# Optimization experiments

Measured on AMD Instinct MI355X. Metric: run time of the kernel, lower is better.

The kernel has to match this reference:

```python
import jax, jax.numpy as jnp
import numpy as np

N = 50000      # nodes
E = 800000     # edges (avg degree 16)
F_IN = 64      # node_features (== GENConv out, so no input projection)
H = 64         # hidden
EXP = 2 * H    # GENConv MLP expansion dim = 128
D2 = F_IN + H  # dense-block concat dim = SAGEConv in = 128
EPS_MSG = 1e-7 # GENConv message eps
BN_EPS = 1e-5


def setup_inputs() -> dict:
    key = jax.random.key(0)
    ks = jax.random.split(key, 16)
    g = lambda k, shape, fan: jax.random.normal(k, shape, jnp.float32) / np.sqrt(fan)
    return {
        "x": jax.random.normal(ks[0], (N, F_IN), jnp.float32),
        "edge_index": jax.random.randint(ks[1], (2, E), 0, N, jnp.int32),
        # GENConv MLP: Linear(64,128) -> BatchNorm(128) -> ReLU -> Linear(128,64)
        "W1": g(ks[2], (H, EXP), H), "b1": jnp.zeros((EXP,), jnp.float32),
        "gamma": jnp.ones((EXP,), jnp.float32), "beta": jnp.zeros((EXP,), jnp.float32),
        "W2": g(ks[3], (EXP, H), EXP), "b2": jnp.zeros((H,), jnp.float32),
        # SAGEConv project Linear(128,128), lin_l Linear(128,64), lin_r Linear(128,64,bias=False)
        "Wp": g(ks[4], (D2, D2), D2), "bp": jnp.zeros((D2,), jnp.float32),
        "Wl": g(ks[5], (D2, H), D2), "bl": jnp.zeros((H,), jnp.float32),
        "Wr": g(ks[6], (D2, H), D2),
        # fc Linear(64,1)
        "Wf": g(ks[7], (H, 1), H), "bf": jnp.zeros((1,), jnp.float32),
    }


def _forward(x, W1, b1, gamma, beta, W2, b2, Wp, bp, Wl, bl, Wr, Wf, bf, src, dst):
    n = x.shape[0]
    # ---- GENConv(aggr='softmax', t=1.0): msg = relu(x_j) + eps -------------
    msg = jax.nn.relu(x[src]) + EPS_MSG                       # [E, H]
    mmax = jax.ops.segment_max(msg, dst, num_segments=n)      # per-dst, per-feature max
    mmax = jax.lax.stop_gradient(jnp.where(jnp.isfinite(mmax), mmax, 0.0))
    e = jnp.exp(msg - mmax[dst])                              # t = 1.0
    denom = jax.ops.segment_sum(e, dst, num_segments=n)
    numer = jax.ops.segment_sum(e * msg, dst, num_segments=n)
    agg = numer / jnp.where(denom > 0, denom, 1.0)            # softmax aggregation
    out = agg + x                                             # residual with x_dst
    # GENConv MLP (BatchNorm in training mode: batch stats, biased var)
    h = out @ W1 + b1
    mu = h.mean(axis=0)
    var = h.var(axis=0)
    h = (h - mu) * jax.lax.rsqrt(var + BN_EPS) * gamma + beta
    h = jax.nn.relu(h) @ W2 + b2                              # [N, H]
    # ---- DeepGCNLayer block='dense': concat input ---------------------------
    x2 = jnp.concatenate([x, h], axis=-1)                     # [N, F_IN+H]
    x2 = jax.nn.sigmoid(x2)                                   # self.relu = Sigmoid()
    # ---- SAGEConv(project=True, aggr=DeepSetsAggregation()==sum) -----------
    xp = jax.nn.relu(x2 @ Wp + bp)                            # projected source feats
    aggr = jax.ops.segment_sum(xp[src], dst, num_segments=n)  # DeepSets w/o nns = sum
    out2 = aggr @ Wl + bl + x2 @ Wr                           # root uses UNprojected x2
    out2 = jax.nn.sigmoid(out2)
    logits = out2 @ Wf + bf                                   # [N, 1]
    probs = jax.nn.sigmoid(logits)                            # training branch
    return probs, logits


def reference(x, edge_index, W1, b1, gamma, beta, W2, b2, Wp, bp, Wl, bl, Wr, Wf, bf):
    src, dst = edge_index[0], edge_index[1]
    return _forward(x, W1, b1, gamma, beta, W2, b2, Wp, bp, Wl, bl, Wr, Wf, bf, src, dst)
```

## Files before the change

kernel.cpp:

```cpp
#include <hip/hip_runtime.h>

#define F_IN 64
#define HID 64
#define EXPD 128
#define D2 128
#define MAXDEG 64
#define NBW 128
#define NB 391
#define BINCAP 2400
#define EPT 32

typedef __attribute__((ext_vector_type(8))) short bf16x8;
typedef __attribute__((ext_vector_type(4))) float f32x4;

__device__ __forceinline__ float sigmoidf_(float x) {
    return 1.0f / (1.0f + __expf(-x));
}
__device__ __forceinline__ unsigned bf16rne_(float f) {
    unsigned u = __float_as_uint(f);
    return (u + 0x7FFFu + ((u >> 16) & 1u)) >> 16;
}
__device__ __forceinline__ float bf16tof_(unsigned u16) {
    return __uint_as_float(u16 << 16);
}

__global__ __launch_bounds__(256) void k_bin(const int* __restrict__ ei,
                                             int* __restrict__ binCount,
                                             unsigned* __restrict__ binned,
                                             const float* __restrict__ x,
                                             unsigned short* __restrict__ x16,
                                             const float* __restrict__ W1,
                                             const float* __restrict__ W2,
                                             const float* __restrict__ Wp,
                                             const float* __restrict__ Wl,
                                             const float* __restrict__ Wr,
                                             short* __restrict__ dst,
                                             int nE, int n, int nbinb) {
    int b = blockIdx.x;
    if (b < nbinb) {
        __shared__ int hist[NB];
        __shared__ int base[NB];
        int tid = threadIdx.x;
        for (int i = tid; i < NB; i += 256) hist[i] = 0;
        __syncthreads();
        unsigned ed[EPT];
        unsigned short rk[EPT];
        int e0 = b * (256 * EPT);
#pragma unroll
        for (int j = 0; j < EPT; ++j) {
            int e = e0 + j * 256 + tid;
            if (e < nE) {
                unsigned s = (unsigned)ei[e];
                unsigned d = (unsigned)ei[nE + e];
                ed[j] = s | (d << 16);
                rk[j] = (unsigned short)atomicAdd(&hist[d >> 7], 1);
            }
        }
        __syncthreads();
        for (int i = tid; i < NB; i += 256) {
            int h = hist[i];
            base[i] = h > 0 ? atomicAdd(&binCount[i], h) : 0;
        }
        __syncthreads();
#pragma unroll
        for (int j = 0; j < EPT; ++j) {
            int e = e0 + j * 256 + tid;
            if (e < nE) {
                int bin = (ed[j] >> 16) >> 7;
                int pos = base[bin] + (int)rk[j];
                if (pos < BINCAP) binned[(size_t)bin * BINCAP + pos] = ed[j];
            }
        }
        return;
    }
    b -= nbinb;
    if (b < 192) {
        int e = b * 256 + threadIdx.x;
        const float* src;
        int K, N, base2;
        if (e < 8192)       { src = W1; K = 64;  N = 128; base2 = 0; }
        else if (e < 16384) { src = W2; K = 128; N = 64;  base2 = 8192; }
        else if (e < 32768) { src = Wp; K = 128; N = 128; base2 = 16384; }
        else if (e < 40960) { src = Wl; K = 128; N = 64;  base2 = 32768; }
        else                { src = Wr; K = 128; N = 64;  base2 = 40960; }
        int le = e - base2;
        int j = le & 7;
        int lane = (le >> 3) & 63;
        int n16 = lane & 15, q = lane >> 4;
        int rest = le >> 9;
        int KC = K / 32;
        int kc = rest % KC, nt = rest / KC;
        int k = kc * 32 + q * 8 + j;
        int col = nt * 16 + n16;
        dst[e] = (short)bf16rne_(src[(size_t)k * N + col]);
        return;
    }
    int i0 = (b - 192) * 1024 + threadIdx.x * 4;
    if (i0 < n * F_IN) {
        float4 v = *(const float4*)(x + i0);
        uint2 pk;
        pk.x = bf16rne_(v.x) | (bf16rne_(v.y) << 16);
        pk.y = bf16rne_(v.z) | (bf16rne_(v.w) << 16);
        *(uint2*)(x16 + i0) = pk;
    }
}

__global__ __launch_bounds__(256) void k_csr(const int* __restrict__ binCount,
                                             const unsigned* __restrict__ binned,
                                             int* __restrict__ counts,
                                             unsigned short* __restrict__ csr, int n) {
    __shared__ unsigned short lcsr[NBW * MAXDEG];
    __shared__ int lcnt[NBW];
    int b = blockIdx.x;
    int tid = threadIdx.x;
    if (tid < NBW) lcnt[tid] = 0;
    __syncthreads();
    int cnt = binCount[b];
    cnt = cnt < BINCAP ? cnt : BINCAP;
    const unsigned* src = binned + (size_t)b * BINCAP;
    for (int i = tid; i < cnt; i += 256) {
        unsigned u = src[i];
        int dl = (int)(u >> 16) - b * NBW;
        int slot = atomicAdd(&lcnt[dl], 1);
        if (slot < MAXDEG) lcsr[dl * MAXDEG + slot] = (unsigned short)(u & 0xFFFF);
    }
    __syncthreads();
    int nodebase = b * NBW;
    if (tid < NBW && nodebase + tid < n) counts[nodebase + tid] = lcnt[tid];
    int nrows = n - nodebase;
    nrows = nrows < NBW ? nrows : NBW;
    int nu4 = nrows * 8;
    uint4* dstrow = (uint4*)(csr + (size_t)nodebase * MAXDEG);
    for (int idx = tid; idx < nu4; idx += 256) dstrow[idx] = ((const uint4*)lcsr)[idx];
}

__global__ __launch_bounds__(256) void k_gengemm1(const unsigned short* __restrict__ x16,
                                                  const int* __restrict__ counts,
                                                  const unsigned short* __restrict__ csr,
                                                  const short* __restrict__ Wf,
                                                  const float* __restrict__ b1,
                                                  unsigned short* __restrict__ h16,
                                                  float* __restrict__ bnsums, int n) {
    __shared__ short As[64 * 64];
    __shared__ float bnred[256];
    const unsigned* x32 = (const unsigned*)x16;
    int tid = threadIdx.x;
    int rblk = blockIdx.x * 64;
    if (tid < 256) bnred[tid] = 0.f;
    int L = tid & 63, w = tid >> 6;
    int H = L >> 5, f2 = L & 31;
    for (int t = 0; t < 16; ++t) {
        int vv = rblk + w * 16 + t;
        int v = vv < n ? vv : n - 1;
        int deg = counts[v];
        deg = deg > MAXDEG ? MAXDEG : deg;
        int idx = 0;
        if (L < deg) idx = (int)csr[(size_t)v * MAXDEG + L];
        float d0 = 0.f, d1 = 0.f, n0 = 0.f, n1 = 0.f;
        int i = 0;
        for (; i + 8 <= deg; i += 8) {
            int sA = __shfl(idx, i + 0 + H, 64);
            int sB = __shfl(idx, i + 2 + H, 64);
            int sC = __shfl(idx, i + 4 + H, 64);
            int sD = __shfl(idx, i + 6 + H, 64);
            unsigned uA = x32[(size_t)sA * 32 + f2];
            unsigned uB = x32[(size_t)sB * 32 + f2];
            unsigned uC = x32[(size_t)sC * 32 + f2];
            unsigned uD = x32[(size_t)sD * 32 + f2];
#pragma unroll
            for (int tt = 0; tt < 4; ++tt) {
                unsigned u = tt == 0 ? uA : tt == 1 ? uB : tt == 2 ? uC : uD;
                float m0 = fmaxf(bf16tof_(u & 0xFFFF), 0.f) + 1e-7f;
                float m1 = fmaxf(bf16tof_(u >> 16), 0.f) + 1e-7f;
                float e0 = __expf(m0), e1 = __expf(m1);
                d0 += e0; d1 += e1;
                n0 = fmaf(e0, m0, n0);
                n1 = fmaf(e1, m1, n1);
            }
        }
        for (; i + 2 <= deg; i += 2) {
            int s = __shfl(idx, i + H, 64);
            unsigned u = x32[(size_t)s * 32 + f2];
            float m0 = fmaxf(bf16tof_(u & 0xFFFF), 0.f) + 1e-7f;
            float m1 = fmaxf(bf16tof_(u >> 16), 0.f) + 1e-7f;
            float e0 = __expf(m0), e1 = __expf(m1);
            d0 += e0; d1 += e1;
            n0 = fmaf(e0, m0, n0);
            n1 = fmaf(e1, m1, n1);
        }
        if (i < deg) {
            int s = __shfl(idx, i, 64);
            if (H == 0) {
                unsigned u = x32[(size_t)s * 32 + f2];
                float m0 = fmaxf(bf16tof_(u & 0xFFFF), 0.f) + 1e-7f;
                float m1 = fmaxf(bf16tof_(u >> 16), 0.f) + 1e-7f;
                float e0 = __expf(m0), e1 = __expf(m1);
                d0 += e0; d1 += e1;
                n0 = fmaf(e0, m0, n0);
                n1 = fmaf(e1, m1, n1);
            }
        }
        d0 += __shfl_xor(d0, 32, 64);
        d1 += __shfl_xor(d1, 32, 64);
        n0 += __shfl_xor(n0, 32, 64);
        n1 += __shfl_xor(n1, 32, 64);
        if (H == 0) {
            float a0 = (deg > 0) ? (n0 / d0) : 0.f;
            float a1 = (deg > 0) ? (n1 / d1) : 0.f;
            unsigned xv = x32[(size_t)v * 32 + f2];
            float r0 = a0 + bf16tof_(xv & 0xFFFF);
            float r1 = a1 + bf16tof_(xv >> 16);
            int q8 = f2 >> 2;
            int j = (2 * f2) & 7;
            int slot = (w * 2 + (q8 >> 2)) * 64 + (q8 & 3) * 16 + t;
            *(unsigned*)(As + slot * 8 + j) = bf16rne_(r0) | (bf16rne_(r1) << 16);
        }
    }
    __syncthreads();
    int q = L >> 4, n16 = L & 15;
    int mt_base = (w & 1) * 2;
    int nt_base = (w >> 1) * 4;
    f32x4 acc[2][4];
#pragma unroll
    for (int mt = 0; mt < 2; ++mt)
#pragma unroll
        for (int nt = 0; nt < 4; ++nt) acc[mt][nt] = (f32x4){0.f, 0.f, 0.f, 0.f};
#pragma unroll
    for (int kc = 0; kc < 2; ++kc) {
        bf16x8 a0 = *(const bf16x8*)(As + (((mt_base + 0) * 2 + kc) * 64 + L) * 8);
        bf16x8 a1 = *(const bf16x8*)(As + (((mt_base + 1) * 2 + kc) * 64 + L) * 8);
#pragma unroll
        for (int nt = 0; nt < 4; ++nt) {
            bf16x8 b = *(const bf16x8*)(Wf + (size_t)(((nt_base + nt) * 2 + kc) * 64 + L) * 8);
            acc[0][nt] = __builtin_amdgcn_mfma_f32_16x16x32_bf16(a0, b, acc[0][nt], 0, 0, 0);
            acc[1][nt] = __builtin_amdgcn_mfma_f32_16x16x32_bf16(a1, b, acc[1][nt], 0, 0, 0);
        }
    }
#pragma unroll
    for (int nt = 0; nt < 4; ++nt) {
        int col = (nt_base + nt) * 16 + n16;
        float bv = b1[col];
        float s = 0.f, s2 = 0.f;
#pragma unroll
        for (int mt = 0; mt < 2; ++mt)
#pragma unroll
            for (int r = 0; r < 4; ++r) {
                int row = rblk + (w & 1) * 32 + mt * 16 + q * 4 + r;
                float hv = acc[mt][nt][r] + bv;
                if (row < n) {
                    h16[(size_t)row * EXPD + col] = (unsigned short)bf16rne_(hv);
                    s += hv;
                    s2 = fmaf(hv, hv, s2);
                }
            }
        s += __shfl_xor(s, 16, 64);
        s += __shfl_xor(s, 32, 64);
        s2 += __shfl_xor(s2, 16, 64);
        s2 += __shfl_xor(s2, 32, 64);
        if (q == 0) {
            atomicAdd(&bnred[col], s);
            atomicAdd(&bnred[128 + col], s2);
        }
    }
    __syncthreads();
    if (tid < 256) atomicAdd(&bnsums[tid], bnred[tid]);
}

__global__ __launch_bounds__(256) void k_mlp2(const unsigned short* __restrict__ h16,
                                              const float* __restrict__ bnsums,
                                              const float* __restrict__ gamma,
                                              const float* __restrict__ beta,
                                              const short* __restrict__ Wf2,
                                              const float* __restrict__ b2,
                                              const unsigned short* __restrict__ x16,
                                              const short* __restrict__ Wfp,
                                              const short* __restrict__ Wfl,
                                              const float* __restrict__ bp,
                                              unsigned short* __restrict__ x2_16,
                                              unsigned short* __restrict__ yp16,
                                              float inv_n, int n) {
    __shared__ short As[128 * 128];
    __shared__ float ssl[256];
    int tid = threadIdx.x;
    int rblk = blockIdx.x * 128;
    if (tid < 128) {
        float mu = bnsums[tid] * inv_n;
        float var = fmaf(-mu, mu, bnsums[128 + tid] * inv_n);
        float rs = rsqrtf(fmaxf(var, 0.f) + 1e-5f);
        float scale = gamma[tid] * rs;
        ssl[tid] = scale;
        ssl[128 + tid] = fmaf(-mu, scale, beta[tid]);
    }
    __syncthreads();
#pragma unroll
    for (int it = 0; it < 8; ++it) {
        int c = it * 256 + tid;
        int rr = c & 127, q8 = c >> 7;
        int gr = rblk + rr;
        gr = gr < n ? gr : n - 1;
        uint4 v = *(const uint4*)(h16 + (size_t)gr * EXPD + q8 * 8);
        float4 sc1 = *(const float4*)(ssl + q8 * 8);
        float4 sc2 = *(const float4*)(ssl + q8 * 8 + 4);
        float4 sh1 = *(const float4*)(ssl + 128 + q8 * 8);
        float4 sh2 = *(const float4*)(ssl + 128 + q8 * 8 + 4);
        float o0 = fmaxf(fmaf(bf16tof_(v.x & 0xFFFF), sc1.x, sh1.x), 0.f);
        float o1 = fmaxf(fmaf(bf16tof_(v.x >> 16),    sc1.y, sh1.y), 0.f);
        float o2 = fmaxf(fmaf(bf16tof_(v.y & 0xFFFF), sc1.z, sh1.z), 0.f);
        float o3 = fmaxf(fmaf(bf16tof_(v.y >> 16),    sc1.w, sh1.w), 0.f);
        float o4 = fmaxf(fmaf(bf16tof_(v.z & 0xFFFF), sc2.x, sh2.x), 0.f);
        float o5 = fmaxf(fmaf(bf16tof_(v.z >> 16),    sc2.y, sh2.y), 0.f);
        float o6 = fmaxf(fmaf(bf16tof_(v.w & 0xFFFF), sc2.z, sh2.z), 0.f);
        float o7 = fmaxf(fmaf(bf16tof_(v.w >> 16),    sc2.w, sh2.w), 0.f);
        uint4 pk;
        pk.x = bf16rne_(o0) | (bf16rne_(o1) << 16);
        pk.y = bf16rne_(o2) | (bf16rne_(o3) << 16);
        pk.z = bf16rne_(o4) | (bf16rne_(o5) << 16);
        pk.w = bf16rne_(o6) | (bf16rne_(o7) << 16);
        int slot = ((rr >> 4) * 4 + (q8 >> 2)) * 64 + (q8 & 3) * 16 + (rr & 15);
        *(uint4*)(As + slot * 8) = pk;
    }
    __syncthreads();
    int L = tid & 63, w = tid >> 6;
    int q = L >> 4, n16 = L & 15;
    f32x4 acc[2][4];
#pragma unroll
    for (int mt = 0; mt < 2; ++mt)
#pragma unroll
        for (int nt = 0; nt < 4; ++nt) acc[mt][nt] = (f32x4){0.f, 0.f, 0.f, 0.f};
#pragma unroll
    for (int kc = 0; kc < 4; ++kc) {
        bf16x8 a0 = *(const bf16x8*)(As + (((w * 2 + 0) * 4 + kc) * 64 + L) * 8);
        bf16x8 a1 = *(const bf16x8*)(As + (((w * 2 + 1) * 4 + kc) * 64 + L) * 8);
#pragma unroll
        for (int nt = 0; nt < 4; ++nt) {
            bf16x8 b = *(const bf16x8*)(Wf2 + (size_t)((nt * 4 + kc) * 64 + L) * 8);
            acc[0][nt] = __builtin_amdgcn_mfma_f32_16x16x32_bf16(a0, b, acc[0][nt], 0, 0, 0);
            acc[1][nt] = __builtin_amdgcn_mfma_f32_16x16x32_bf16(a1, b, acc[1][nt], 0, 0, 0);
        }
    }
    __syncthreads();
#pragma unroll
    for (int it = 0; it < 8; ++it) {
        int i = it * 256 + tid;
        int rr = i >> 4, c4 = i & 15;
        int gr = rblk + rr;
        int grc = gr < n ? gr : n - 1;
        uint2 xv = ((const uint2*)x16)[(size_t)grc * 16 + c4];
        float s0 = sigmoidf_(bf16tof_(xv.x & 0xFFFF));
        float s1 = sigmoidf_(bf16tof_(xv.x >> 16));
        float s2 = sigmoidf_(bf16tof_(xv.y & 0xFFFF));
        float s3 = sigmoidf_(bf16tof_(xv.y >> 16));
        uint2 pk;
        pk.x = bf16rne_(s0) | (bf16rne_(s1) << 16);
        pk.y = bf16rne_(s2) | (bf16rne_(s3) << 16);
        if (gr < n) *(uint2*)(x2_16 + (size_t)gr * D2 + c4 * 4) = pk;
        int q8 = c4 >> 1, j = (c4 & 1) * 4;
        int slot = ((rr >> 4) * 4 + (q8 >> 2)) * 64 + (q8 & 3) * 16 + (rr & 15);
        *(uint2*)(As + slot * 8 + j) = pk;
    }
#pragma unroll
    for (int nt = 0; nt < 4; ++nt) {
        int col = nt * 16 + n16;
        float bv = b2[col];
        int kk = 64 + col;
        int q8b = kk >> 3, jb = kk & 7;
#pragma unroll
        for (int mt = 0; mt < 2; ++mt)
#pragma unroll
            for (int r = 0; r < 4; ++r) {
                int rr2 = w * 32 + mt * 16 + q * 4 + r;
                int row = rblk + rr2;
                unsigned sv = bf16rne_(sigmoidf_(acc[mt][nt][r] + bv));
                if (row < n)
                    x2_16[(size_t)row * D2 + 64 + col] = (unsigned short)sv;
                int slot = ((rr2 >> 4) * 4 + (q8b >> 2)) * 64 + (q8b & 3) * 16 + (rr2 & 15);
                As[slot * 8 + jb] = (short)sv;
            }
    }
    __syncthreads();
    f32x4 accp[2][8];
#pragma unroll
    for (int mt = 0; mt < 2; ++mt)
#pragma unroll
        for (int nt = 0; nt < 8; ++nt) accp[mt][nt] = (f32x4){0.f, 0.f, 0.f, 0.f};
#pragma unroll
    for (int kc = 0; kc < 4; ++kc) {
        bf16x8 a0 = *(const bf16x8*)(As + (((w * 2 + 0) * 4 + kc) * 64 + L) * 8);
        bf16x8 a1 = *(const bf16x8*)(As + (((w * 2 + 1) * 4 + kc) * 64 + L) * 8);
#pragma unroll
        for (int nt = 0; nt < 8; ++nt) {
            bf16x8 b = *(const bf16x8*)(Wfp + (size_t)((nt * 4 + kc) * 64 + L) * 8);
            accp[0][nt] = __builtin_amdgcn_mfma_f32_16x16x32_bf16(a0, b, accp[0][nt], 0, 0, 0);
            accp[1][nt] = __builtin_amdgcn_mfma_f32_16x16x32_bf16(a1, b, accp[1][nt], 0, 0, 0);
        }
    }
#pragma unroll
    for (int nt = 0; nt < 8; ++nt) {
        int col = nt * 16 + n16;
        float bv = bp[col];
        int q8b = col >> 3, jb = col & 7;
#pragma unroll
        for (int mt = 0; mt < 2; ++mt)
#pragma unroll
            for (int r = 0; r < 4; ++r) {
                int rr2 = (w * 2 + mt) * 16 + q * 4 + r;
                float xv = fmaxf(accp[mt][nt][r] + bv, 0.f);
                int slot = ((rr2 >> 4) * 4 + (q8b >> 2)) * 64 + (q8b & 3) * 16 + (rr2 & 15);
                As[slot * 8 + jb] = (short)bf16rne_(xv);
            }
    }
    f32x4 acc2[2][4];
#pragma unroll
    for (int mt = 0; mt < 2; ++mt)
#pragma unroll
        for (int nt = 0; nt < 4; ++nt) acc2[mt][nt] = (f32x4){0.f, 0.f, 0.f, 0.f};
#pragma unroll
    for (int kc = 0; kc < 4; ++kc) {
        bf16x8 a0 = *(const bf16x8*)(As + (((w * 2 + 0) * 4 + kc) * 64 + L) * 8);
        bf16x8 a1 = *(const bf16x8*)(As + (((w * 2 + 1) * 4 + kc) * 64 + L) * 8);
#pragma unroll
        for (int nt = 0; nt < 4; ++nt) {
            bf16x8 b = *(const bf16x8*)(Wfl + (size_t)((nt * 4 + kc) * 64 + L) * 8);
            acc2[0][nt] = __builtin_amdgcn_mfma_f32_16x16x32_bf16(a0, b, acc2[0][nt], 0, 0, 0);
            acc2[1][nt] = __builtin_amdgcn_mfma_f32_16x16x32_bf16(a1, b, acc2[1][nt], 0, 0, 0);
        }
    }
#pragma unroll
    for (int nt = 0; nt < 4; ++nt) {
        int col = nt * 16 + n16;
#pragma unroll
        for (int mt = 0; mt < 2; ++mt)
#pragma unroll
            for (int r = 0; r < 4; ++r) {
                int row = rblk + (w * 2 + mt) * 16 + q * 4 + r;
                if (row < n)
                    yp16[(size_t)row * HID + col] =
                        (unsigned short)bf16rne_(acc2[mt][nt][r]);
            }
    }
}

__global__ __launch_bounds__(256) void k_sage(const unsigned short* __restrict__ yp16,
                                              const int* __restrict__ counts,
                                              const unsigned short* __restrict__ csr,
                                              unsigned short* __restrict__ aggr16, int n) {
    const unsigned* yp32 = (const unsigned*)yp16;
    int wid = threadIdx.x >> 6;
    int lane = threadIdx.x & 63;
    int H = lane >> 5, f2 = lane & 31;
    int v = blockIdx.x * 4 + wid;
    if (v >= n) return;
    int deg = counts[v];
    deg = deg > MAXDEG ? MAXDEG : deg;
    int idx = 0;
    if (lane < deg) idx = (int)csr[(size_t)v * MAXDEG + lane];
    float a0 = 0.f, a1 = 0.f;
    int i = 0;
    for (; i + 8 <= deg; i += 8) {
        int sA = __shfl(idx, i + 0 + H, 64);
        int sB = __shfl(idx, i + 2 + H, 64);
        int sC = __shfl(idx, i + 4 + H, 64);
        int sD = __shfl(idx, i + 6 + H, 64);
        unsigned uA = yp32[(size_t)sA * 32 + f2];
        unsigned uB = yp32[(size_t)sB * 32 + f2];
        unsigned uC = yp32[(size_t)sC * 32 + f2];
        unsigned uD = yp32[(size_t)sD * 32 + f2];
        a0 += bf16tof_(uA & 0xFFFF) + bf16tof_(uB & 0xFFFF) +
              bf16tof_(uC & 0xFFFF) + bf16tof_(uD & 0xFFFF);
        a1 += bf16tof_(uA >> 16) + bf16tof_(uB >> 16) +
              bf16tof_(uC >> 16) + bf16tof_(uD >> 16);
    }
    for (; i + 2 <= deg; i += 2) {
        int s = __shfl(idx, i + H, 64);
        unsigned u = yp32[(size_t)s * 32 + f2];
        a0 += bf16tof_(u & 0xFFFF);
        a1 += bf16tof_(u >> 16);
    }
    if (i < deg) {
        int s = __shfl(idx, i, 64);
        if (H == 0) {
            unsigned u = yp32[(size_t)s * 32 + f2];
            a0 += bf16tof_(u & 0xFFFF);
            a1 += bf16tof_(u >> 16);
        }
    }
    a0 += __shfl_xor(a0, 32, 64);
    a1 += __shfl_xor(a1, 32, 64);
    if (H == 0)
        ((unsigned*)aggr16)[(size_t)v * 32 + f2] = bf16rne_(a0) | (bf16rne_(a1) << 16);
}

__global__ __launch_bounds__(256) void k_final(const unsigned short* __restrict__ aggr16,
                                               const unsigned short* __restrict__ x2_16,
                                               const short* __restrict__ Wfr,
                                               const float* __restrict__ bl,
                                               const float* __restrict__ Wfv,
                                               const float* __restrict__ bf,
                                               float* __restrict__ out, int n) {
    __shared__ short As[128 * 128];
    int tid = threadIdx.x;
    int rblk = blockIdx.x * 128;
#pragma unroll
    for (int it = 0; it < 8; ++it) {
        int c = it * 256 + tid;
        int rr = c & 127, q8 = c >> 7;
        int gr = rblk + rr;
        gr = gr < n ? gr : n - 1;
        uint4 v = *(const uint4*)(x2_16 + (size_t)gr * D2 + q8 * 8);
        int slot = ((rr >> 4) * 4 + (q8 >> 2)) * 64 + (q8 & 3) * 16 + (rr & 15);
        *(uint4*)(As + slot * 8) = v;
    }
    __syncthreads();
    int L = tid & 63, w = tid >> 6;
    int q = L >> 4, n16 = L & 15;
    int mt_base = w * 2;
    f32x4 acc[2][4];
#pragma unroll
    for (int mt = 0; mt < 2; ++mt)
#pragma unroll
        for (int nt = 0; nt < 4; ++nt) acc[mt][nt] = (f32x4){0.f, 0.f, 0.f, 0.f};
#pragma unroll
    for (int kc = 0; kc < 4; ++kc) {
        bf16x8 a0 = *(const bf16x8*)(As + (((mt_base + 0) * 4 + kc) * 64 + L) * 8);
        bf16x8 a1 = *(const bf16x8*)(As + (((mt_base + 1) * 4 + kc) * 64 + L) * 8);
#pragma unroll
        for (int nt = 0; nt < 4; ++nt) {
            bf16x8 b = *(const bf16x8*)(Wfr + (size_t)((nt * 4 + kc) * 64 + L) * 8);
            acc[0][nt] = __builtin_amdgcn_mfma_f32_16x16x32_bf16(a0, b, acc[0][nt], 0, 0, 0);
            acc[1][nt] = __builtin_amdgcn_mfma_f32_16x16x32_bf16(a1, b, acc[1][nt], 0, 0, 0);
        }
    }
    float blv[4], wfv[4];
#pragma unroll
    for (int nt = 0; nt < 4; ++nt) {
        blv[nt] = bl[nt * 16 + n16];
        wfv[nt] = Wfv[nt * 16 + n16];
    }
    float bf0 = bf[0];
#pragma unroll
    for (int mt = 0; mt < 2; ++mt)
#pragma unroll
        for (int r = 0; r < 4; ++r) {
            int row = rblk + w * 32 + mt * 16 + q * 4 + r;
            int rowc = row < n ? row : n - 1;
            float t = 0.f;
#pragma unroll
            for (int nt = 0; nt < 4; ++nt) {
                float ag = bf16tof_(aggr16[(size_t)rowc * HID + nt * 16 + n16]);
                t = fmaf(sigmoidf_(acc[mt][nt][r] + blv[nt] + ag), wfv[nt], t);
            }
            t += __shfl_xor(t, 1, 64);
            t += __shfl_xor(t, 2, 64);
            t += __shfl_xor(t, 4, 64);
            t += __shfl_xor(t, 8, 64);
            if (n16 == 0 && row < n) {
                float lg = t + bf0;
                out[row] = sigmoidf_(lg);
                out[n + row] = lg;
            }
        }
}

extern "C" void kernel_launch(void* const* d_in, const int* in_sizes, int n_in,
                              void* d_out, int out_size, void* d_ws, size_t ws_size,
                              hipStream_t stream) {
    const float* x     = (const float*)d_in[0];
    const int*   ei    = (const int*)d_in[1];
    const float* W1    = (const float*)d_in[2];
    const float* b1    = (const float*)d_in[3];
    const float* gamma = (const float*)d_in[4];
    const float* beta  = (const float*)d_in[5];
    const float* W2    = (const float*)d_in[6];
    const float* b2    = (const float*)d_in[7];
    const float* Wp    = (const float*)d_in[8];
    const float* bp    = (const float*)d_in[9];
    const float* Wl    = (const float*)d_in[10];
    const float* bl    = (const float*)d_in[11];
    const float* Wr    = (const float*)d_in[12];
    const float* Wfv   = (const float*)d_in[13];
    const float* bf    = (const float*)d_in[14];
    const int n = in_sizes[0] / F_IN;
    const int e = in_sizes[1] / 2;

    char* ws = (char*)d_ws;
    size_t off = 0;
    auto alloc = [&](size_t bytes) -> void* {
        void* p = (void*)(ws + off);
        off += (bytes + 255) & ~(size_t)255;
        return p;
    };
    float*          bnsums   = (float*)alloc(256 * 4 + NB * 4);
    int*            binCount = (int*)((char*)bnsums + 1024);
    int*            counts   = (int*)alloc((size_t)n * 4);
    unsigned short* csr      = (unsigned short*)alloc((size_t)n * MAXDEG * 2);
    unsigned*       binned   = (unsigned*)alloc((size_t)NB * BINCAP * 4);
    unsigned short* x16      = (unsigned short*)alloc((size_t)n * F_IN * 2);
    unsigned short* h16      = (unsigned short*)alloc((size_t)n * EXPD * 2);
    unsigned short* x2_16    = (unsigned short*)alloc((size_t)n * D2 * 2);
    unsigned short* yp16     = (unsigned short*)alloc((size_t)n * HID * 2);
    unsigned short* aggr16   = (unsigned short*)alloc((size_t)n * HID * 2);
    short*          wfrag    = (short*)alloc(49152 * 2);

    float* out = (float*)d_out;
    const int nb64  = (n + 63) / 64;
    const int nb128 = (n + 127) / 128;
    const int nb4   = (n + 3) / 4;
    const int nbinb = (e + 256 * EPT - 1) / (256 * EPT);
    const int nfp = nbinb + 192 + ((n * F_IN + 1023) / 1024);

    hipMemsetAsync(bnsums, 0, 1024 + NB * 4, stream);

    k_bin<<<nfp, 256, 0, stream>>>(ei, binCount, binned, x, x16, W1, W2, Wp, Wl,
                                   Wr, wfrag, e, n, nbinb);
    k_csr<<<NB, 256, 0, stream>>>(binCount, binned, counts, csr, n);
    k_gengemm1<<<nb64, 256, 0, stream>>>(x16, counts, csr, wfrag, b1, h16,
                                         bnsums, n);
    k_mlp2<<<nb128, 256, 0, stream>>>(h16, bnsums, gamma, beta, wfrag + 8192, b2,
                                      x16, wfrag + 16384, wfrag + 32768, bp,
                                      x2_16, yp16, 1.0f / (float)n, n);
    k_sage<<<nb4, 256, 0, stream>>>(yp16, counts, csr, aggr16, n);
    k_final<<<nb128, 256, 0, stream>>>(aggr16, x2_16, wfrag + 40960, bl, Wfv, bf,
                                       out, n);
}
```

Baseline: 246.1 us.

## Split fused softmax-gather and GEMM1 into separate per-node gather kernel

Splits the fused GENConv softmax aggregation and first MLP GEMM kernel into two kernels. The gather kernel now gives each wavefront a single node, so there are many more blocks and more memory-level parallelism, instead of each wave walking 16 nodes in sequence. The result goes to a new bf16 global buffer, which the GEMM kernel then loads into shared memory. The trade-off is an extra kernel launch and a round trip of an N×64 bf16 buffer through global memory.

```diff
diff --git a/kernel.cpp b/kernel.cpp
--- a/kernel.cpp
+++ b/kernel.cpp
@@ -134,52 +134,55 @@
     for (int idx = tid; idx < nu4; idx += 256) dstrow[idx] = ((const uint4*)lcsr)[idx];
 }
 
-__global__ __launch_bounds__(256) void k_gengemm1(const unsigned short* __restrict__ x16,
-                                                  const int* __restrict__ counts,
-                                                  const unsigned short* __restrict__ csr,
-                                                  const short* __restrict__ Wf,
-                                                  const float* __restrict__ b1,
-                                                  unsigned short* __restrict__ h16,
-                                                  float* __restrict__ bnsums, int n) {
-    __shared__ short As[64 * 64];
-    __shared__ float bnred[256];
+__global__ __launch_bounds__(256) void k_gen(const unsigned short* __restrict__ x16,
+                                             const int* __restrict__ counts,
+                                             const unsigned short* __restrict__ csr,
+                                             unsigned short* __restrict__ gen16, int n) {
     const unsigned* x32 = (const unsigned*)x16;
-    int tid = threadIdx.x;
-    int rblk = blockIdx.x * 64;
-    if (tid < 256) bnred[tid] = 0.f;
-    int L = tid & 63, w = tid >> 6;
-    int H = L >> 5, f2 = L & 31;
-    for (int t = 0; t < 16; ++t) {
-        int vv = rblk + w * 16 + t;
-        int v = vv < n ? vv : n - 1;
-        int deg = counts[v];
-        deg = deg > MAXDEG ? MAXDEG : deg;
-        int idx = 0;
-        if (L < deg) idx = (int)csr[(size_t)v * MAXDEG + L];
-        float d0 = 0.f, d1 = 0.f, n0 = 0.f, n1 = 0.f;
-        int i = 0;
-        for (; i + 8 <= deg; i += 8) {
-            int sA = __shfl(idx, i + 0 + H, 64);
-            int sB = __shfl(idx, i + 2 + H, 64);
-            int sC = __shfl(idx, i + 4 + H, 64);
-            int sD = __shfl(idx, i + 6 + H, 64);
-            unsigned uA = x32[(size_t)sA * 32 + f2];
-            unsigned uB = x32[(size_t)sB * 32 + f2];
-            unsigned uC = x32[(size_t)sC * 32 + f2];
-            unsigned uD = x32[(size_t)sD * 32 + f2];
-#pragma unroll
-            for (int tt = 0; tt < 4; ++tt) {
-                unsigned u = tt == 0 ? uA : tt == 1 ? uB : tt == 2 ? uC : uD;
-                float m0 = fmaxf(bf16tof_(u & 0xFFFF), 0.f) + 1e-7f;
-                float m1 = fmaxf(bf16tof_(u >> 16), 0.f) + 1e-7f;
-                float e0 = __expf(m0), e1 = __expf(m1);
-                d0 += e0; d1 += e1;
-                n0 = fmaf(e0, m0, n0);
-                n1 = fmaf(e1, m1, n1);
-            }
-        }
-        for (; i + 2 <= deg; i += 2) {
-            int s = __shfl(idx, i + H, 64);
+    int wid = threadIdx.x >> 6;
+    int lane = threadIdx.x & 63;
+    int H = lane >> 5, f2 = lane & 31;
+    int v = blockIdx.x * 4 + wid;
+    if (v >= n) return;
+    int deg = counts[v];
+    deg = deg > MAXDEG ? MAXDEG : deg;
+    int idx = 0;
+    if (lane < deg) idx = (int)csr[(size_t)v * MAXDEG + lane];
+    float d0 = 0.f, d1 = 0.f, n0 = 0.f, n1 = 0.f;
+    int i = 0;
+    for (; i + 8 <= deg; i += 8) {
+        int sA = __shfl(idx, i + 0 + H, 64);
+        int sB = __shfl(idx, i + 2 + H, 64);
+        int sC = __shfl(idx, i + 4 + H, 64);
+        int sD = __shfl(idx, i + 6 + H, 64);
+        unsigned uA = x32[(size_t)sA * 32 + f2];
+        unsigned uB = x32[(size_t)sB * 32 + f2];
+        unsigned uC = x32[(size_t)sC * 32 + f2];
+        unsigned uD = x32[(size_t)sD * 32 + f2];
+#pragma unroll
+        for (int t = 0; t < 4; ++t) {
+            unsigned u = t == 0 ? uA : t == 1 ? uB : t == 2 ? uC : uD;
+            float m0 = fmaxf(bf16tof_(u & 0xFFFF), 0.f) + 1e-7f;
+            float m1 = fmaxf(bf16tof_(u >> 16), 0.f) + 1e-7f;
+            float e0 = __expf(m0), e1 = __expf(m1);
+            d0 += e0; d1 += e1;
+            n0 = fmaf(e0, m0, n0);
+            n1 = fmaf(e1, m1, n1);
+        }
+    }
+    for (; i + 2 <= deg; i += 2) {
+        int s = __shfl(idx, i + H, 64);
+        unsigned u = x32[(size_t)s * 32 + f2];
+        float m0 = fmaxf(bf16tof_(u & 0xFFFF), 0.f) + 1e-7f;
+        float m1 = fmaxf(bf16tof_(u >> 16), 0.f) + 1e-7f;
+        float e0 = __expf(m0), e1 = __expf(m1);
+        d0 += e0; d1 += e1;
+        n0 = fmaf(e0, m0, n0);
+        n1 = fmaf(e1, m1, n1);
+    }
+    if (i < deg) {
+        int s = __shfl(idx, i, 64);
+        if (H == 0) {
             unsigned u = x32[(size_t)s * 32 + f2];
             float m0 = fmaxf(bf16tof_(u & 0xFFFF), 0.f) + 1e-7f;
             float m1 = fmaxf(bf16tof_(u >> 16), 0.f) + 1e-7f;
@@ -188,35 +191,44 @@
             n0 = fmaf(e0, m0, n0);
             n1 = fmaf(e1, m1, n1);
         }
-        if (i < deg) {
-            int s = __shfl(idx, i, 64);
-            if (H == 0) {
-                unsigned u = x32[(size_t)s * 32 + f2];
-                float m0 = fmaxf(bf16tof_(u & 0xFFFF), 0.f) + 1e-7f;
-                float m1 = fmaxf(bf16tof_(u >> 16), 0.f) + 1e-7f;
-                float e0 = __expf(m0), e1 = __expf(m1);
-                d0 += e0; d1 += e1;
-                n0 = fmaf(e0, m0, n0);
-                n1 = fmaf(e1, m1, n1);
-            }
-        }
-        d0 += __shfl_xor(d0, 32, 64);
-        d1 += __shfl_xor(d1, 32, 64);
-        n0 += __shfl_xor(n0, 32, 64);
-        n1 += __shfl_xor(n1, 32, 64);
-        if (H == 0) {
-            float a0 = (deg > 0) ? (n0 / d0) : 0.f;
-            float a1 = (deg > 0) ? (n1 / d1) : 0.f;
-            unsigned xv = x32[(size_t)v * 32 + f2];
-            float r0 = a0 + bf16tof_(xv & 0xFFFF);
-            float r1 = a1 + bf16tof_(xv >> 16);
-            int q8 = f2 >> 2;
-            int j = (2 * f2) & 7;
-            int slot = (w * 2 + (q8 >> 2)) * 64 + (q8 & 3) * 16 + t;
-            *(unsigned*)(As + slot * 8 + j) = bf16rne_(r0) | (bf16rne_(r1) << 16);
-        }
-    }
-    __syncthreads();
+    }
+    d0 += __shfl_xor(d0, 32, 64);
+    d1 += __shfl_xor(d1, 32, 64);
+    n0 += __shfl_xor(n0, 32, 64);
+    n1 += __shfl_xor(n1, 32, 64);
+    if (H == 0) {
+        float a0 = (deg > 0) ? (n0 / d0) : 0.f;
+        float a1 = (deg > 0) ? (n1 / d1) : 0.f;
+        unsigned xv = x32[(size_t)v * 32 + f2];
+        float r0 = a0 + bf16tof_(xv & 0xFFFF);
+        float r1 = a1 + bf16tof_(xv >> 16);
+        ((unsigned*)gen16)[(size_t)v * 32 + f2] =
+            bf16rne_(r0) | (bf16rne_(r1) << 16);
+    }
+}
+
+__global__ __launch_bounds__(256) void k_gemm1(const unsigned short* __restrict__ gen16,
+                                               const short* __restrict__ Wf,
+                                               const float* __restrict__ b1,
+                                               unsigned short* __restrict__ h16,
+                                               float* __restrict__ bnsums, int n) {
+    __shared__ short As[64 * 64];
+    __shared__ float bnred[256];
+    int tid = threadIdx.x;
+    int rblk = blockIdx.x * 64;
+    if (tid < 256) bnred[tid] = 0.f;
+#pragma unroll
+    for (int it = 0; it < 2; ++it) {
+        int c = it * 256 + tid;
+        int rr = c & 63, q8 = c >> 6;
+        int gr = rblk + rr;
+        gr = gr < n ? gr : n - 1;
+        uint4 v = *(const uint4*)(gen16 + (size_t)gr * F_IN + q8 * 8);
+        int slot = ((rr >> 4) * 2 + (q8 >> 2)) * 64 + (q8 & 3) * 16 + (rr & 15);
+        *(uint4*)(As + slot * 8) = v;
+    }
+    __syncthreads();
+    int L = tid & 63, w = tid >> 6;
     int q = L >> 4, n16 = L & 15;
     int mt_base = (w & 1) * 2;
     int nt_base = (w >> 1) * 4;
@@ -595,6 +607,7 @@
     unsigned short* csr      = (unsigned short*)alloc((size_t)n * MAXDEG * 2);
     unsigned*       binned   = (unsigned*)alloc((size_t)NB * BINCAP * 4);
     unsigned short* x16      = (unsigned short*)alloc((size_t)n * F_IN * 2);
+    unsigned short* gen16    = (unsigned short*)alloc((size_t)n * F_IN * 2);
     unsigned short* h16      = (unsigned short*)alloc((size_t)n * EXPD * 2);
     unsigned short* x2_16    = (unsigned short*)alloc((size_t)n * D2 * 2);
     unsigned short* yp16     = (unsigned short*)alloc((size_t)n * HID * 2);
@@ -613,8 +626,8 @@
     k_bin<<<nfp, 256, 0, stream>>>(ei, binCount, binned, x, x16, W1, W2, Wp, Wl,
                                    Wr, wfrag, e, n, nbinb);
     k_csr<<<NB, 256, 0, stream>>>(binCount, binned, counts, csr, n);
-    k_gengemm1<<<nb64, 256, 0, stream>>>(x16, counts, csr, wfrag, b1, h16,
-                                         bnsums, n);
+    k_gen<<<nb4, 256, 0, stream>>>(x16, counts, csr, gen16, n);
+    k_gemm1<<<nb64, 256, 0, stream>>>(gen16, wfrag, b1, h16, bnsums, n);
     k_mlp2<<<nb128, 256, 0, stream>>>(h16, bnsums, gamma, beta, wfrag + 8192, b2,
                                       x16, wfrag + 16384, wfrag + 32768, bp,
                                       x2_16, yp16, 1.0f / (float)n, n);
```

Measured after the change: 234.8 us. 4.6% less time.
